# Optimization experiments

Hardware: AMD Instinct MI355X
Metric: run time of the kernel (lower is better)

## Reference

```python
import jax, jax.numpy as jnp
import numpy as np

INPUT_DIM = 512
OUTPUT_DIM = 2048
GAMMA = 0.5
N_ROWS = 65536


def setup_inputs() -> dict:
    key = jax.random.key(0)
    kx, kw, kb = jax.random.split(key, 3)
    input_tensor = jax.random.normal(kx, (N_ROWS, INPUT_DIM), dtype=jnp.float32)
    # RBFSampler.fit: random_weights_ = sqrt(2*gamma) * N(0,1), random_offset_ ~ U(0, 2pi)
    W = jnp.sqrt(2.0 * GAMMA) * jax.random.normal(kw, (INPUT_DIM, OUTPUT_DIM), dtype=jnp.float32)
    b = jax.random.uniform(kb, (OUTPUT_DIM,), dtype=jnp.float32, minval=0.0, maxval=2.0 * np.pi)
    return {"input_tensor": input_tensor, "W": W, "b": b}


def reference(input_tensor, W, b):
    # RBFSampler.transform: cos(X @ W + b) * sqrt(2 / n_components)
    proj = input_tensor @ W + b  # [N, output_dim]
    scale = jnp.sqrt(jnp.asarray(2.0 / OUTPUT_DIM, dtype=proj.dtype))
    return jnp.cos(proj) * scale
```

## Files before the change

kernel.cpp:

```cpp
#include <hip/hip_runtime.h>

typedef __bf16 bf16x8 __attribute__((ext_vector_type(8)));
typedef float  f32x4  __attribute__((ext_vector_type(4)));
typedef int    i32x4  __attribute__((ext_vector_type(4)));
typedef char   c16    __attribute__((ext_vector_type(16)));

constexpr int M_ROWS = 65536;
constexpr int N_COLS = 2048;
constexpr int K_DIM  = 512;
constexpr int NKQ    = 8;
constexpr int MBQ    = 512;
constexpr int NBQ    = 16;

constexpr size_t AQ_OFF  = (65536 + 2048) * 4;
constexpr size_t AQ_SZ   = (size_t)MBQ * NKQ * 16384;
constexpr size_t WQ_OFF  = AQ_OFF + AQ_SZ;
constexpr size_t WQ_SZ   = (size_t)NBQ * NKQ * 16384;
constexpr size_t NEEDQ   = WQ_OFF + WQ_SZ;

__device__ __forceinline__ unsigned short f2bf(float f){
  unsigned int u = __float_as_uint(f);
  u += 0x7FFFu + ((u >> 16) & 1u);
  return (unsigned short)(u >> 16);
}
__device__ __forceinline__ float bf2f(unsigned short h){
  return __uint_as_float(((unsigned int)h) << 16);
}
__device__ __forceinline__ void split4(const float4& v, ushort4& h, ushort4& l){
  h.x = f2bf(v.x); l.x = f2bf(v.x - bf2f(h.x));
  h.y = f2bf(v.y); l.y = f2bf(v.y - bf2f(h.y));
  h.z = f2bf(v.z); l.z = f2bf(v.z - bf2f(h.z));
  h.w = f2bf(v.w); l.w = f2bf(v.w - bf2f(h.w));
}

__device__ __forceinline__ void gl_lds16(const void* g, void* l){
  __builtin_amdgcn_global_load_lds(
      (const __attribute__((address_space(1))) unsigned int*)g,
      (__attribute__((address_space(3))) unsigned int*)l, 16, 0, 0);
}

constexpr float INV2PI = 0.15915494309189535f;
__device__ __forceinline__ float cos_scaled(float v){
  float rev = v * INV2PI;
  rev -= floorf(rev);
  return 0.03125f * __builtin_amdgcn_cosf(rev);
}

__device__ __forceinline__ void q2(float x, float inv, char& o1, char& o2){
  float t1 = x * inv;
  float r1 = rintf(t1);
  float r2 = fminf(rintf((t1 - r1) * 256.0f), 127.0f);
  o1 = (char)(int)r1;
  o2 = (char)(int)r2;
}

__global__ void pack_xq(const float* __restrict__ X, char* __restrict__ AQ,
                        float* __restrict__ sXo){
  const int bid = blockIdx.x;
  const int t = threadIdx.x;
  const int rl = t >> 3, seg = t & 7;
  const int grow = bid * 32 + rl;
  const float* src = X + (size_t)grow * K_DIM + seg * 64;
  f32x4 v[16];
  #pragma unroll
  for (int i = 0; i < 16; ++i)
    v[i] = __builtin_nontemporal_load(reinterpret_cast<const f32x4*>(src) + i);
  float m = 0.f;
  #pragma unroll
  for (int i = 0; i < 16; ++i)
    m = fmaxf(m, fmaxf(fmaxf(fabsf(v[i].x), fabsf(v[i].y)),
                       fmaxf(fabsf(v[i].z), fabsf(v[i].w))));
  m = fmaxf(m, __shfl_xor(m, 1));
  m = fmaxf(m, __shfl_xor(m, 2));
  m = fmaxf(m, __shfl_xor(m, 4));
  m = fmaxf(m, 1e-10f);
  if (seg == 0) sXo[grow] = m * (1.0f / 127.0f);
  const float inv = 127.0f / m;

  const int mb = bid >> 2;
  const int rowt = (bid & 3) * 32 + rl;
  const int i_ = rowt >> 4, r_ = rowt & 15;
  char* tb = AQ + (size_t)(mb * NKQ + seg) * 16384;
  #pragma unroll
  for (int q = 0; q < 4; ++q){
    c16 o1, o2;
    #pragma unroll
    for (int u = 0; u < 4; ++u){
      f32x4 xv = v[q * 4 + u];
      #pragma unroll
      for (int w = 0; w < 4; ++w){
        char a, b; q2(xv[w], inv, a, b);
        o1[u * 4 + w] = a; o2[u * 4 + w] = b;
      }
    }
    int c = i_ * 64 + q * 16 + r_;
    *reinterpret_cast<c16*>(tb + c * 16)        = o1;
    *reinterpret_cast<c16*>(tb + 8192 + c * 16) = o2;
  }
}

__global__ void scale_w(const float* __restrict__ W, float* __restrict__ sWo){
  __shared__ float red[8][32];
  int t = threadIdx.x, nl = t & 31, kq = t >> 5;
  int n = blockIdx.x * 32 + nl;
  float m = 0.f;
  for (int k = kq * 64; k < kq * 64 + 64; ++k)
    m = fmaxf(m, fabsf(W[(size_t)k * N_COLS + n]));
  red[kq][nl] = m;
  __syncthreads();
  if (kq == 0){
    #pragma unroll
    for (int u = 1; u < 8; ++u) m = fmaxf(m, red[u][nl]);
    sWo[n] = fmaxf(m, 1e-10f) * (1.0f / 127.0f);
  }
}

__global__ void pack_wq(const float* __restrict__ W, const float* __restrict__ sW,
                        char* __restrict__ WQ){
  __shared__ float tf[64][132];
  const int nb = blockIdx.x, kt = blockIdx.y, t = threadIdx.x;
  const int kr = t >> 2, nq = t & 3;
  #pragma unroll
  for (int it = 0; it < 8; ++it){
    f32x4 v4 = *reinterpret_cast<const f32x4*>(
        W + (size_t)(kt * 64 + kr) * N_COLS + nb * 128 + nq * 32 + it * 4);
    *reinterpret_cast<f32x4*>(&tf[kr][nq * 32 + it * 4]) = v4;
  }
  __syncthreads();
  char* tb = WQ + (size_t)(nb * NKQ + kt) * 16384;
  #pragma unroll
  for (int cc = 0; cc < 2; ++cc){
    int c = t + cc * 256;
    int jj = c >> 6, q = (c >> 4) & 3, fc = c & 15;
    int col_local = (jj >> 2) * 64 + fc * 4 + (jj & 3);
    float inv = 1.0f / sW[nb * 128 + col_local];
    c16 o1, o2;
    #pragma unroll
    for (int e = 0; e < 16; ++e){
      char a, b; q2(tf[q * 16 + e][col_local], inv, a, b);
      o1[e] = a; o2[e] = b;
    }
    *reinterpret_cast<c16*>(tb + c * 16)        = o1;
    *reinterpret_cast<c16*>(tb + 8192 + c * 16) = o2;
  }
}

#define MFMAI(a,b,c) __builtin_amdgcn_mfma_i32_16x16x64_i8(a,b,c,0,0,0)

__launch_bounds__(256, 2)
__global__ void rbf_gemm_i8(const char* __restrict__ AQ, const char* __restrict__ WQ,
                            const float* __restrict__ sX, const float* __restrict__ sW,
                            const float* __restrict__ bvec, float* __restrict__ out){
  __shared__ __align__(16) char smem[2 * 16384];

  int orig = blockIdx.x;
  int wgid = (orig & 7) * 1024 + (orig >> 3);
  int mb = wgid >> 4, nb = wgid & 15;
  int m0 = mb * 128, n0 = nb * 128;

  int tid = threadIdx.x, lane = tid & 63, wid = tid >> 6;
  int wm = wid >> 1, wn = wid & 1;
  int r = lane & 15, g = lane >> 4;

  const char* abase = AQ + (size_t)mb * NKQ * 16384;
  const char* bbase = WQ + (size_t)nb * NKQ * 16384;
  const int bsoff = wid * 1024 + lane * 16;
  const int bdoff = wid * 1024;

  int aoffs[4], boffs[4];
  #pragma unroll
  for (int i = 0; i < 4; ++i) aoffs[i] = (wm * 4 + i) * 1024 + lane * 16;
  #pragma unroll
  for (int j = 0; j < 4; ++j) boffs[j] = (wn * 4 + j) * 1024 + lane * 16;

  i32x4 accm[4][4], accc[4][4];
  #pragma unroll
  for (int i = 0; i < 4; ++i)
    #pragma unroll
    for (int j = 0; j < 4; ++j){
      accm[i][j] = (i32x4){0,0,0,0};
      accc[i][j] = (i32x4){0,0,0,0};
    }

  i32x4 a1A[4], a2A[4], a1B[4], a2B[4];

  #pragma unroll
  for (int i = 0; i < 4; ++i){
    a1A[i] = *reinterpret_cast<const i32x4*>(abase + aoffs[i]);
    a2A[i] = *reinterpret_cast<const i32x4*>(abase + 8192 + aoffs[i]);
  }
  #pragma unroll
  for (int it = 0; it < 4; ++it)
    gl_lds16(bbase + it * 4096 + bsoff, smem + it * 4096 + bdoff);
  __syncthreads();

  #pragma unroll 1
  for (int kt = 0; kt < NKQ; kt += 2){
    {
      const char* bb = bbase + (size_t)(kt + 1) * 16384;
      #pragma unroll
      for (int it = 0; it < 4; ++it)
        gl_lds16(bb + it * 4096 + bsoff, smem + 16384 + it * 4096 + bdoff);
      const char* ab = abase + (size_t)(kt + 1) * 16384;
      #pragma unroll
      for (int i = 0; i < 4; ++i){
        a1B[i] = *reinterpret_cast<const i32x4*>(ab + aoffs[i]);
        a2B[i] = *reinterpret_cast<const i32x4*>(ab + 8192 + aoffs[i]);
      }
      const char* SB = smem;
      #pragma unroll
      for (int j = 0; j < 4; ++j){
        i32x4 b1 = *reinterpret_cast<const i32x4*>(SB + boffs[j]);
        i32x4 b2 = *reinterpret_cast<const i32x4*>(SB + 8192 + boffs[j]);
        #pragma unroll
        for (int i = 0; i < 4; ++i){
          accm[i][j] = MFMAI(a1A[i], b1, accm[i][j]);
          accc[i][j] = MFMAI(a1A[i], b2, accc[i][j]);
          accc[i][j] = MFMAI(a2A[i], b1, accc[i][j]);
        }
      }
      __syncthreads();
    }
    {
      if (kt + 2 < NKQ){
        const char* bb = bbase + (size_t)(kt + 2) * 16384;
        #pragma unroll
        for (int it = 0; it < 4; ++it)
          gl_lds16(bb + it * 4096 + bsoff, smem + it * 4096 + bdoff);
        const char* ab = abase + (size_t)(kt + 2) * 16384;
        #pragma unroll
        for (int i = 0; i < 4; ++i){
          a1A[i] = *reinterpret_cast<const i32x4*>(ab + aoffs[i]);
          a2A[i] = *reinterpret_cast<const i32x4*>(ab + 8192 + aoffs[i]);
        }
      }
      const char* SB = smem + 16384;
      #pragma unroll
      for (int j = 0; j < 4; ++j){
        i32x4 b1 = *reinterpret_cast<const i32x4*>(SB + boffs[j]);
        i32x4 b2 = *reinterpret_cast<const i32x4*>(SB + 8192 + boffs[j]);
        #pragma unroll
        for (int i = 0; i < 4; ++i){
          accm[i][j] = MFMAI(a1B[i], b1, accm[i][j]);
          accc[i][j] = MFMAI(a1B[i], b2, accc[i][j]);
          accc[i][j] = MFMAI(a2B[i], b1, accc[i][j]);
        }
      }
      __syncthreads();
    }
  }

  int colb = n0 + wn * 64 + r * 4;
  f32x4 sw4 = *reinterpret_cast<const f32x4*>(sW + colb);
  f32x4 bv  = *reinterpret_cast<const f32x4*>(bvec + colb);
  #pragma unroll
  for (int i = 0; i < 4; ++i){
    int rowb = m0 + wm * 64 + i * 16 + g * 4;
    f32x4 sx4 = *reinterpret_cast<const f32x4*>(sX + rowb);
    #pragma unroll
    for (int p = 0; p < 4; ++p){
      float sx = sx4[p];
      f32x4 o;
      o.x = cos_scaled(fmaf(sx * sw4.x,
              (float)accm[i][0][p] + (float)accc[i][0][p] * 0.00390625f, bv.x));
      o.y = cos_scaled(fmaf(sx * sw4.y,
              (float)accm[i][1][p] + (float)accc[i][1][p] * 0.00390625f, bv.y));
      o.z = cos_scaled(fmaf(sx * sw4.z,
              (float)accm[i][2][p] + (float)accc[i][2][p] * 0.00390625f, bv.z));
      o.w = cos_scaled(fmaf(sx * sw4.w,
              (float)accm[i][3][p] + (float)accc[i][3][p] * 0.00390625f, bv.w));
      __builtin_nontemporal_store(o,
          reinterpret_cast<f32x4*>(out + (size_t)(rowb + p) * N_COLS + colb));
    }
  }
}

#define MFMA_(a,b,c) __builtin_amdgcn_mfma_f32_16x16x32_bf16(a,b,c,0,0,0)
constexpr int LDSK = 40;
constexpr int SEC  = 128 * LDSK;
__launch_bounds__(256, 2)
__global__ void rbf_gemm_nows(const float* __restrict__ X, const float* __restrict__ W,
                              const float* __restrict__ bvec, float* __restrict__ out){
  __shared__ __align__(16) unsigned short smem[4 * SEC];
  int orig = blockIdx.x;
  int wgid = (orig & 7) * (int)(gridDim.x >> 3) + (orig >> 3);
  int mb = wgid >> 4, nb = wgid & 15;
  int m0 = mb * 128, n0 = nb * 128;
  int tid = threadIdx.x, lane = tid & 63, wid = tid >> 6;
  int wm = wid >> 1, wn = wid & 1;
  int r = lane & 15, g = lane >> 4;

  const float* asrc[4]; int alofs[4]; float4 ra[4];
  const float* wsrc[4]; int wnq4[4]; int wkr[4]; float4 rw[4];
  #pragma unroll
  for (int i = 0; i < 4; ++i){
    int c = tid + i * 256;
    int row = c >> 3, q = c & 7;
    asrc[i]  = X + (size_t)(m0 + row) * K_DIM + q * 4;
    alofs[i] = row * LDSK + q * 4;
  }
  #pragma unroll
  for (int i = 0; i < 4; ++i) ra[i] = *reinterpret_cast<const float4*>(asrc[i]);
  #pragma unroll
  for (int i = 0; i < 4; ++i){
    int c = tid + i * 256;
    int kr = c >> 5, nq = c & 31;
    wsrc[i] = W + (size_t)kr * N_COLS + n0 + nq * 4;
    wkr[i] = kr; wnq4[i] = nq * 4;
  }
  #pragma unroll
  for (int i = 0; i < 4; ++i) rw[i] = *reinterpret_cast<const float4*>(wsrc[i]);

  f32x4 acc[4][4];
  #pragma unroll
  for (int i = 0; i < 4; ++i)
    #pragma unroll
    for (int j = 0; j < 4; ++j) acc[i][j] = (f32x4){0.f,0.f,0.f,0.f};

  int aoff[4], boff[4];
  #pragma unroll
  for (int i = 0; i < 4; ++i) aoff[i] = (wm*64 + i*16 + r) * LDSK + g * 8;
  #pragma unroll
  for (int j = 0; j < 4; ++j) boff[j] = (wn*64 + j*16 + r) * LDSK + g * 8;

  #pragma unroll 1
  for (int kt = 0; kt < 16; ++kt){
    __syncthreads();
    #pragma unroll
    for (int i = 0; i < 4; ++i){
      ushort4 h, l;
      split4(ra[i], h, l);
      *reinterpret_cast<ushort4*>(&smem[alofs[i]])       = h;
      *reinterpret_cast<ushort4*>(&smem[SEC + alofs[i]]) = l;
    }
    #pragma unroll
    for (int i = 0; i < 4; ++i){
      float vv[4] = {rw[i].x, rw[i].y, rw[i].z, rw[i].w};
      #pragma unroll
      for (int w2 = 0; w2 < 4; ++w2){
        unsigned short h = f2bf(vv[w2]);
        unsigned short l = f2bf(vv[w2] - bf2f(h));
        int n = wnq4[i] + w2;
        smem[2*SEC + n*LDSK + wkr[i]] = h;
        smem[3*SEC + n*LDSK + wkr[i]] = l;
      }
    }
    if (kt < 15){
      #pragma unroll
      for (int i = 0; i < 4; ++i)
        ra[i] = *reinterpret_cast<const float4*>(asrc[i] + (kt+1)*32);
      #pragma unroll
      for (int i = 0; i < 4; ++i)
        rw[i] = *reinterpret_cast<const float4*>(wsrc[i] + (size_t)(kt+1)*32*N_COLS);
    }
    __syncthreads();
    bf16x8 ah[4], al[4], bh[4], bl[4];
    #pragma unroll
    for (int i = 0; i < 4; ++i){
      ah[i] = *reinterpret_cast<const bf16x8*>(&smem[aoff[i]]);
      al[i] = *reinterpret_cast<const bf16x8*>(&smem[SEC + aoff[i]]);
    }
    #pragma unroll
    for (int j = 0; j < 4; ++j){
      bh[j] = *reinterpret_cast<const bf16x8*>(&smem[2*SEC + boff[j]]);
      bl[j] = *reinterpret_cast<const bf16x8*>(&smem[3*SEC + boff[j]]);
    }
    #pragma unroll
    for (int i = 0; i < 4; ++i){
      #pragma unroll
      for (int j = 0; j < 4; ++j){
        acc[i][j] = MFMA_(ah[i], bh[j], acc[i][j]);
        acc[i][j] = MFMA_(al[i], bh[j], acc[i][j]);
        acc[i][j] = MFMA_(ah[i], bl[j], acc[i][j]);
      }
    }
  }

  float bvv[4];
  #pragma unroll
  for (int j = 0; j < 4; ++j) bvv[j] = bvec[n0 + wn*64 + j*16 + r];
  #pragma unroll
  for (int i = 0; i < 4; ++i){
    #pragma unroll
    for (int j = 0; j < 4; ++j){
      int col = n0 + wn*64 + j*16 + r;
      #pragma unroll
      for (int p = 0; p < 4; ++p){
        int row = m0 + wm*64 + i*16 + g*4 + p;
        out[(size_t)row * N_COLS + col] = cos_scaled(acc[i][j][p] + bvv[j]);
      }
    }
  }
}

extern "C" void kernel_launch(void* const* d_in, const int* in_sizes, int n_in,
                              void* d_out, int out_size, void* d_ws, size_t ws_size,
                              hipStream_t stream){
  const float* X = (const float*)d_in[0];
  const float* W = (const float*)d_in[1];
  const float* b = (const float*)d_in[2];
  float* out = (float*)d_out;
  char* ws = (char*)d_ws;

  if (ws && ws_size >= NEEDQ){
    float* sX = (float*)ws;
    float* sW = (float*)(ws + 65536 * 4);
    char*  AQ = ws + AQ_OFF;
    char*  WQ = ws + WQ_OFF;
    pack_xq<<<2048, 256, 0, stream>>>(X, AQ, sX);
    scale_w<<<64, 256, 0, stream>>>(W, sW);
    pack_wq<<<dim3(NBQ, NKQ), 256, 0, stream>>>(W, sW, WQ);
    rbf_gemm_i8<<<8192, 256, 0, stream>>>(AQ, WQ, sX, sW, b, out);
  } else {
    rbf_gemm_nows<<<8192, 256, 0, stream>>>(X, W, b, out);
  }
}
```

Before: 315.0 us.

## Stage two K-tiles of W per LDS buffer and drain loads before barriers

Restructures the main GEMM loop so each double-buffered LDS stage holds two K-tiles (32 KB) of quantized W, halving the number of barriers per block. The A fragments for both K-tiles are loaded directly into registers at the start of each iteration rather than prefetched one step ahead. An explicit vmcnt(0) wait plus a sched_barrier now precedes each barrier so the direct global-to-LDS copies are complete. In exchange, LDS use doubles to 64 KB per block, which may limit occupancy. The A loads are also no longer overlapped with the previous stage's MFMAs, so their latency can be exposed.

```diff
diff --git a/kernel.cpp b/kernel.cpp
--- a/kernel.cpp
+++ b/kernel.cpp
@@ -146,12 +146,14 @@
 }
 
 #define MFMAI(a,b,c) __builtin_amdgcn_mfma_i32_16x16x64_i8(a,b,c,0,0,0)
+#define DRAIN_BAR() { asm volatile("s_waitcnt vmcnt(0)" ::: "memory"); \
+                      __builtin_amdgcn_sched_barrier(0); __syncthreads(); }
 
 __launch_bounds__(256, 2)
 __global__ void rbf_gemm_i8(const char* __restrict__ AQ, const char* __restrict__ WQ,
                             const float* __restrict__ sX, const float* __restrict__ sW,
                             const float* __restrict__ bvec, float* __restrict__ out){
-  __shared__ __align__(16) char smem[2 * 16384];
+  __shared__ __align__(16) char smem[2 * 32768];
 
   int orig = blockIdx.x;
   int wgid = (orig & 7) * 1024 + (orig >> 3);
@@ -182,72 +184,51 @@
       accc[i][j] = (i32x4){0,0,0,0};
     }
 
-  i32x4 a1A[4], a2A[4], a1B[4], a2B[4];
-
-  #pragma unroll
-  for (int i = 0; i < 4; ++i){
-    a1A[i] = *reinterpret_cast<const i32x4*>(abase + aoffs[i]);
-    a2A[i] = *reinterpret_cast<const i32x4*>(abase + 8192 + aoffs[i]);
-  }
-  #pragma unroll
-  for (int it = 0; it < 4; ++it)
+  #pragma unroll
+  for (int it = 0; it < 8; ++it)
     gl_lds16(bbase + it * 4096 + bsoff, smem + it * 4096 + bdoff);
-  __syncthreads();
+  DRAIN_BAR();
 
   #pragma unroll 1
-  for (int kt = 0; kt < NKQ; kt += 2){
-    {
-      const char* bb = bbase + (size_t)(kt + 1) * 16384;
-      #pragma unroll
-      for (int it = 0; it < 4; ++it)
-        gl_lds16(bb + it * 4096 + bsoff, smem + 16384 + it * 4096 + bdoff);
-      const char* ab = abase + (size_t)(kt + 1) * 16384;
+  for (int t = 0; t < 4; ++t){
+    const char* SB = smem + (t & 1) * 32768;
+
+    i32x4 a1[2][4], a2[2][4];
+    #pragma unroll
+    for (int kq = 0; kq < 2; ++kq){
+      const char* ab = abase + (size_t)(2 * t + kq) * 16384;
       #pragma unroll
       for (int i = 0; i < 4; ++i){
-        a1B[i] = *reinterpret_cast<const i32x4*>(ab + aoffs[i]);
-        a2B[i] = *reinterpret_cast<const i32x4*>(ab + 8192 + aoffs[i]);
-      }
-      const char* SB = smem;
+        a1[kq][i] = *reinterpret_cast<const i32x4*>(ab + aoffs[i]);
+        a2[kq][i] = *reinterpret_cast<const i32x4*>(ab + 8192 + aoffs[i]);
+      }
+    }
+
+    if (t < 3){
+      const char* s = bbase + (size_t)(t + 1) * 32768;
+      char* d = smem + ((t + 1) & 1) * 32768;
+      #pragma unroll
+      for (int it = 0; it < 8; ++it)
+        gl_lds16(s + it * 4096 + bsoff, d + it * 4096 + bdoff);
+    }
+
+    #pragma unroll
+    for (int kq = 0; kq < 2; ++kq){
+      const char* SBk = SB + kq * 16384;
       #pragma unroll
       for (int j = 0; j < 4; ++j){
-        i32x4 b1 = *reinterpret_cast<const i32x4*>(SB + boffs[j]);
-        i32x4 b2 = *reinterpret_cast<const i32x4*>(SB + 8192 + boffs[j]);
+        i32x4 b1 = *reinterpret_cast<const i32x4*>(SBk + boffs[j]);
+        i32x4 b2 = *reinterpret_cast<const i32x4*>(SBk + 8192 + boffs[j]);
         #pragma unroll
         for (int i = 0; i < 4; ++i){
-          accm[i][j] = MFMAI(a1A[i], b1, accm[i][j]);
-          accc[i][j] = MFMAI(a1A[i], b2, accc[i][j]);
-          accc[i][j] = MFMAI(a2A[i], b1, accc[i][j]);
+          accm[i][j] = MFMAI(a1[kq][i], b1, accm[i][j]);
+          accc[i][j] = MFMAI(a1[kq][i], b2, accc[i][j]);
+          accc[i][j] = MFMAI(a2[kq][i], b1, accc[i][j]);
         }
       }
-      __syncthreads();
-    }
-    {
-      if (kt + 2 < NKQ){
-        const char* bb = bbase + (size_t)(kt + 2) * 16384;
-        #pragma unroll
-        for (int it = 0; it < 4; ++it)
-          gl_lds16(bb + it * 4096 + bsoff, smem + it * 4096 + bdoff);
-        const char* ab = abase + (size_t)(kt + 2) * 16384;
-        #pragma unroll
-        for (int i = 0; i < 4; ++i){
-          a1A[i] = *reinterpret_cast<const i32x4*>(ab + aoffs[i]);
-          a2A[i] = *reinterpret_cast<const i32x4*>(ab + 8192 + aoffs[i]);
-        }
-      }
-      const char* SB = smem + 16384;
-      #pragma unroll
-      for (int j = 0; j < 4; ++j){
-        i32x4 b1 = *reinterpret_cast<const i32x4*>(SB + boffs[j]);
-        i32x4 b2 = *reinterpret_cast<const i32x4*>(SB + 8192 + boffs[j]);
-        #pragma unroll
-        for (int i = 0; i < 4; ++i){
-          accm[i][j] = MFMAI(a1B[i], b1, accm[i][j]);
-          accc[i][j] = MFMAI(a1B[i], b2, accc[i][j]);
-          accc[i][j] = MFMAI(a2B[i], b1, accc[i][j]);
-        }
-      }
-      __syncthreads();
-    }
+    }
+
+    DRAIN_BAR();
   }
 
   int colb = n0 + wn * 64 + r * 4;
```

Measured after the change: 320.9 us. About the same (+1.9%).

## Halve GEMM tile width to 128x64 and raise occupancy to four blocks per CU

Applied to the files above, without the earlier changes.

The int8 GEMM tile shrinks from 128x128 to 128x64 per workgroup. Each wave now owns 32 rows by 64 columns, which halves the accumulator and A-register footprint and halves LDS use, so launch bounds can allow 4 blocks per CU, and the grid doubles to 16384. Barriers now explicitly drain vmcnt before syncing, which makes completion of the global-to-LDS loads explicit. The trade-off is that A tiles are reloaded twice as often across workgroups, reducing arithmetic intensity, in exchange for more latency hiding from higher occupancy.

```diff
diff --git a/kernel.cpp b/kernel.cpp
--- a/kernel.cpp
+++ b/kernel.cpp
@@ -146,64 +146,64 @@
 }
 
 #define MFMAI(a,b,c) __builtin_amdgcn_mfma_i32_16x16x64_i8(a,b,c,0,0,0)
-
-__launch_bounds__(256, 2)
+#define DRAIN_BAR() { asm volatile("s_waitcnt vmcnt(0)" ::: "memory"); \
+                      __builtin_amdgcn_sched_barrier(0); __syncthreads(); }
+
+__launch_bounds__(256, 4)
 __global__ void rbf_gemm_i8(const char* __restrict__ AQ, const char* __restrict__ WQ,
                             const float* __restrict__ sX, const float* __restrict__ sW,
                             const float* __restrict__ bvec, float* __restrict__ out){
-  __shared__ __align__(16) char smem[2 * 16384];
+  __shared__ __align__(16) char smem[2 * 8192];
 
   int orig = blockIdx.x;
-  int wgid = (orig & 7) * 1024 + (orig >> 3);
-  int mb = wgid >> 4, nb = wgid & 15;
-  int m0 = mb * 128, n0 = nb * 128;
+  int wgid = (orig & 7) * 2048 + (orig >> 3);
+  int mb = wgid >> 5, nb2 = wgid & 31;
+  int nb = nb2 >> 1, wn2 = nb2 & 1;
 
   int tid = threadIdx.x, lane = tid & 63, wid = tid >> 6;
-  int wm = wid >> 1, wn = wid & 1;
   int r = lane & 15, g = lane >> 4;
 
   const char* abase = AQ + (size_t)mb * NKQ * 16384;
-  const char* bbase = WQ + (size_t)nb * NKQ * 16384;
-  const int bsoff = wid * 1024 + lane * 16;
-  const int bdoff = wid * 1024;
-
-  int aoffs[4], boffs[4];
-  #pragma unroll
-  for (int i = 0; i < 4; ++i) aoffs[i] = (wm * 4 + i) * 1024 + lane * 16;
-  #pragma unroll
-  for (int j = 0; j < 4; ++j) boffs[j] = (wn * 4 + j) * 1024 + lane * 16;
-
-  i32x4 accm[4][4], accc[4][4];
-  #pragma unroll
-  for (int i = 0; i < 4; ++i)
+  const char* bbase = WQ + ((size_t)nb * NKQ) * 16384 + wn2 * 4096;
+  const int soff = wid * 1024 + lane * 16;
+  const int doff = wid * 1024;
+
+  int aoffs[2];
+  #pragma unroll
+  for (int i = 0; i < 2; ++i) aoffs[i] = (wid * 2 + i) * 1024 + lane * 16;
+  int boffs[4];
+  #pragma unroll
+  for (int j = 0; j < 4; ++j) boffs[j] = j * 1024 + lane * 16;
+
+  i32x4 accm[2][4], accc[2][4];
+  #pragma unroll
+  for (int i = 0; i < 2; ++i)
     #pragma unroll
     for (int j = 0; j < 4; ++j){
       accm[i][j] = (i32x4){0,0,0,0};
       accc[i][j] = (i32x4){0,0,0,0};
     }
 
-  i32x4 a1A[4], a2A[4], a1B[4], a2B[4];
-
-  #pragma unroll
-  for (int i = 0; i < 4; ++i){
+  i32x4 a1A[2], a2A[2], a1B[2], a2B[2];
+
+  #pragma unroll
+  for (int i = 0; i < 2; ++i){
     a1A[i] = *reinterpret_cast<const i32x4*>(abase + aoffs[i]);
     a2A[i] = *reinterpret_cast<const i32x4*>(abase + 8192 + aoffs[i]);
   }
-  #pragma unroll
-  for (int it = 0; it < 4; ++it)
-    gl_lds16(bbase + it * 4096 + bsoff, smem + it * 4096 + bdoff);
-  __syncthreads();
+  gl_lds16(bbase + soff, smem + doff);
+  gl_lds16(bbase + 8192 + soff, smem + 4096 + doff);
+  DRAIN_BAR();
 
   #pragma unroll 1
   for (int kt = 0; kt < NKQ; kt += 2){
     {
       const char* bb = bbase + (size_t)(kt + 1) * 16384;
-      #pragma unroll
-      for (int it = 0; it < 4; ++it)
-        gl_lds16(bb + it * 4096 + bsoff, smem + 16384 + it * 4096 + bdoff);
+      gl_lds16(bb + soff, smem + 8192 + doff);
+      gl_lds16(bb + 8192 + soff, smem + 12288 + doff);
       const char* ab = abase + (size_t)(kt + 1) * 16384;
       #pragma unroll
-      for (int i = 0; i < 4; ++i){
+      for (int i = 0; i < 2; ++i){
         a1B[i] = *reinterpret_cast<const i32x4*>(ab + aoffs[i]);
         a2B[i] = *reinterpret_cast<const i32x4*>(ab + 8192 + aoffs[i]);
       }
@@ -211,51 +211,50 @@
       #pragma unroll
       for (int j = 0; j < 4; ++j){
         i32x4 b1 = *reinterpret_cast<const i32x4*>(SB + boffs[j]);
-        i32x4 b2 = *reinterpret_cast<const i32x4*>(SB + 8192 + boffs[j]);
+        i32x4 b2 = *reinterpret_cast<const i32x4*>(SB + 4096 + boffs[j]);
         #pragma unroll
-        for (int i = 0; i < 4; ++i){
+        for (int i = 0; i < 2; ++i){
           accm[i][j] = MFMAI(a1A[i], b1, accm[i][j]);
           accc[i][j] = MFMAI(a1A[i], b2, accc[i][j]);
           accc[i][j] = MFMAI(a2A[i], b1, accc[i][j]);
         }
       }
-      __syncthreads();
+      DRAIN_BAR();
     }
     {
       if (kt + 2 < NKQ){
         const char* bb = bbase + (size_t)(kt + 2) * 16384;
-        #pragma unroll
-        for (int it = 0; it < 4; ++it)
-          gl_lds16(bb + it * 4096 + bsoff, smem + it * 4096 + bdoff);
+        gl_lds16(bb + soff, smem + doff);
+        gl_lds16(bb + 8192 + soff, smem + 4096 + doff);
         const char* ab = abase + (size_t)(kt + 2) * 16384;
         #pragma unroll
-        for (int i = 0; i < 4; ++i){
+        for (int i = 0; i < 2; ++i){
           a1A[i] = *reinterpret_cast<const i32x4*>(ab + aoffs[i]);
           a2A[i] = *reinterpret_cast<const i32x4*>(ab + 8192 + aoffs[i]);
         }
       }
-      const char* SB = smem + 16384;
+      const char* SB = smem + 8192;
       #pragma unroll
       for (int j = 0; j < 4; ++j){
         i32x4 b1 = *reinterpret_cast<const i32x4*>(SB + boffs[j]);
-        i32x4 b2 = *reinterpret_cast<const i32x4*>(SB + 8192 + boffs[j]);
+        i32x4 b2 = *reinterpret_cast<const i32x4*>(SB + 4096 + boffs[j]);
         #pragma unroll
-        for (int i = 0; i < 4; ++i){
+        for (int i = 0; i < 2; ++i){
           accm[i][j] = MFMAI(a1B[i], b1, accm[i][j]);
           accc[i][j] = MFMAI(a1B[i], b2, accc[i][j]);
           accc[i][j] = MFMAI(a2B[i], b1, accc[i][j]);
         }
       }
-      __syncthreads();
-    }
-  }
-
-  int colb = n0 + wn * 64 + r * 4;
+      DRAIN_BAR();
+    }
+  }
+
+  int colb = nb2 * 64 + r * 4;
   f32x4 sw4 = *reinterpret_cast<const f32x4*>(sW + colb);
   f32x4 bv  = *reinterpret_cast<const f32x4*>(bvec + colb);
   #pragma unroll
-  for (int i = 0; i < 4; ++i){
-    int rowb = m0 + wm * 64 + i * 16 + g * 4;
+  for (int i = 0; i < 2; ++i){
+    int rowb = mb * 128 + wid * 32 + i * 16 + g * 4;
     f32x4 sx4 = *reinterpret_cast<const f32x4*>(sX + rowb);
     #pragma unroll
     for (int p = 0; p < 4; ++p){
@@ -410,7 +409,7 @@
     pack_xq<<<2048, 256, 0, stream>>>(X, AQ, sX);
     scale_w<<<64, 256, 0, stream>>>(W, sW);
     pack_wq<<<dim3(NBQ, NKQ), 256, 0, stream>>>(W, sW, WQ);
-    rbf_gemm_i8<<<8192, 256, 0, stream>>>(AQ, WQ, sX, sW, b, out);
+    rbf_gemm_i8<<<16384, 256, 0, stream>>>(AQ, WQ, sX, sW, b, out);
   } else {
     rbf_gemm_nows<<<8192, 256, 0, stream>>>(X, W, b, out);
   }
```

New measurement: 311.2 us. Within noise of the previous version (-1.2%).
